# Performance work log

Measured on AMD Instinct MI355X. Metric: run time of the kernel, lower is better.

The kernel has to match this reference:

```python
import jax, jax.numpy as jnp
import numpy as np
from jax.scipy.special import digamma

K_NEIGHBOURS = 5  # matches init_kwargs nNeighbours


def setup_inputs() -> dict:
    key = jax.random.key(0)
    k1, k2 = jax.random.split(key)
    x = jax.random.normal(k1, (2, 2, 64, 64), dtype=jnp.float32)
    y = jax.random.normal(k2, (2, 2, 64, 64), dtype=jnp.float32)
    return {"x": x, "y": y}


def _knn_mi(x, y, k):
    # KSG k-NN mutual information estimator, channel-wise.
    B, C, H, W = x.shape
    BC, HW = B * C, H * W
    xv = x.reshape(BC, HW)
    yv = y.reshape(BC, HW)
    # Pairwise L1 (scalar -> abs diff) distance matrices: (BC, HW, HW)
    dx = jnp.abs(xv[:, :, None] - xv[:, None, :])
    dy = jnp.abs(yv[:, :, None] - yv[:, None, :])
    # Joint-space Chebyshev distance (max over the two marginals)
    z = jnp.maximum(dx, dy)
    # eps = (k+1)-th smallest joint distance per point (includes self-distance 0),
    # matching torch .topk(k+1, largest=False).values[..., -1:]
    neg_smallest = jax.lax.top_k(-z, k + 1)[0]       # (BC, HW, k+1), descending in -z
    eps = -neg_smallest[:, :, -1:]                    # (BC, HW, 1)
    # Marginal neighbor counts with strict < eps (self included, as in torch code)
    nx = jnp.sum(dx < eps, axis=-1).astype(jnp.float32)  # (BC, HW)
    ny = jnp.sum(dy < eps, axis=-1).astype(jnp.float32)
    const = digamma(jnp.float32(k)) + digamma(jnp.float32(HW))
    mi = const - jnp.mean(digamma(nx) + digamma(ny), axis=-1)  # (BC,)
    return jnp.maximum(mi.reshape(B, C), 0.0)


def reference(x, y):
    return _knn_mi(x, y, K_NEIGHBOURS)
```

## Files before the change

### kernel.cpp

```cpp
#include <hip/hip_runtime.h>
#include <math.h>

#define HW 4096
#define NCH 4
#define TPB 256
#define ROWS_PER_BLOCK 16
#define BLOCKS_PER_CH 256
#define NBLOCKS (NCH * BLOCKS_PER_CH)
#define KNN 5
#define WIN 512

#define NBINS 512
#define BLO   (-6.0f)
#define BDELTA 0.0234375f
#define BINV  (512.0f / 12.0f)
#define SLOP  1e-5f
#define INFT  3.4e38f

#define WS_BXY   16384
#define WS_BY    32768
#define WS_PREF  49152
#define WS_PART  57344

__device__ __forceinline__ int binOf(float v) {
    int b = (int)floorf((v - BLO) * BINV);
    return min(max(b, 0), NBINS - 1);
}

__device__ __forceinline__ float digammaf_dev(float x) {
    float r = 0.f;
    while (x < 6.f) { r -= 1.f / x; x += 1.f; }
    float f = 1.f / x, f2 = f * f;
    return logf(x) - 0.5f * f
         - f2 * (1.f / 12.f - f2 * (1.f / 120.f - f2 * (1.f / 252.f))) + r;
}

__device__ __forceinline__ void insert6(float (&s)[6], float d) {
    float n0 = fminf(s[0], d);
    float n1 = __builtin_amdgcn_fmed3f(s[0], s[1], d);
    float n2 = __builtin_amdgcn_fmed3f(s[1], s[2], d);
    float n3 = __builtin_amdgcn_fmed3f(s[2], s[3], d);
    float n4 = __builtin_amdgcn_fmed3f(s[3], s[4], d);
    float n5 = __builtin_amdgcn_fmed3f(s[4], s[5], d);
    s[0] = n0; s[1] = n1; s[2] = n2; s[3] = n3; s[4] = n4; s[5] = n5;
}

__global__ __launch_bounds__(256) void knnmi_bucketize(const float* __restrict__ x,
                                                       const float* __restrict__ y,
                                                       float* __restrict__ ws) {
    __shared__ int h[NBINS];
    const int c    = blockIdx.x >> 1;
    const int side = blockIdx.x & 1;
    const int t    = threadIdx.x;
    const float* src  = (side == 0 ? x : y) + c * HW;
    const float* ysrc = y + c * HW;
    int* pref = (int*)ws + WS_PREF + (side ? NCH * (NBINS + 1) : 0) + c * (NBINS + 1);

    for (int i = t; i < NBINS; i += 256) h[i] = 0;
    __syncthreads();

    float vx[16], vy[16];
    int bn[16];
#pragma unroll
    for (int k = 0; k < 16; ++k) {
        int i = t + k * 256;
        float v = src[i];
        vx[k] = v;
        vy[k] = (side == 0) ? ysrc[i] : 0.f;
        bn[k] = binOf(v);
        atomicAdd(&h[bn[k]], 1);
    }
    __syncthreads();

    if (t < 64) {
        int sinc[8];
        {
            int c0 = h[t * 8 + 0];
            sinc[0] = c0;
#pragma unroll
            for (int j = 1; j < 8; ++j) sinc[j] = sinc[j - 1] + h[t * 8 + j];
        }
        int tot = sinc[7], inc = tot;
#pragma unroll
        for (int off = 1; off < 64; off <<= 1) {
            int u = __shfl_up(inc, off);
            if (t >= off) inc += u;
        }
        int ex = inc - tot;
#pragma unroll
        for (int j = 0; j < 8; ++j) {
            int st = ex + (j ? sinc[j - 1] : 0);
            h[t * 8 + j]    = st;
            pref[t * 8 + j] = st;
        }
        if (t == 63) pref[NBINS] = HW;
    }
    __syncthreads();

    if (side == 0) {
        float* bxx = ws + c * HW;
        float* bxy = ws + WS_BXY + c * HW;
#pragma unroll
        for (int k = 0; k < 16; ++k) {
            int pos = atomicAdd(&h[bn[k]], 1);
            bxx[pos] = vx[k];
            bxy[pos] = vy[k];
        }
    } else {
        float* by = ws + WS_BY + c * HW;
#pragma unroll
        for (int k = 0; k < 16; ++k) {
            int pos = atomicAdd(&h[bn[k]], 1);
            by[pos] = vx[k];
        }
    }
}

__global__ __launch_bounds__(TPB) void knnmi_rows(float* __restrict__ ws) {
    __shared__ float2 sxy[HW];
    __shared__ float  ys[HW];
    __shared__ int pfx[NBINS + 1], pfy[NBINS + 1];
    __shared__ float red[ROWS_PER_BLOCK];

    const int c  = blockIdx.x >> 8;
    const int rb = blockIdx.x & 255;
    const float* bxx = ws + c * HW;
    const float* bxy = ws + WS_BXY + c * HW;
    const float* by  = ws + WS_BY  + c * HW;
    const int* prefx = (const int*)ws + WS_PREF + c * (NBINS + 1);
    const int* prefy = (const int*)ws + WS_PREF + NCH * (NBINS + 1) + c * (NBINS + 1);

    for (int i = threadIdx.x; i < HW / 4; i += TPB) {
        float4 xv = ((const float4*)bxx)[i];
        float4 yv = ((const float4*)bxy)[i];
        ((float4*)sxy)[2 * i]     = make_float4(xv.x, yv.x, xv.y, yv.y);
        ((float4*)sxy)[2 * i + 1] = make_float4(xv.z, yv.z, xv.w, yv.w);
        ((float4*)ys)[i] = ((const float4*)by)[i];
    }
    for (int i = threadIdx.x; i <= NBINS; i += TPB) {
        pfx[i] = prefx[i];
        pfy[i] = prefy[i];
    }
    __syncthreads();

    const int wv   = threadIdx.x >> 6;
    const int lane = threadIdx.x & 63;
    const int l    = lane & 15;
    const int g    = lane >> 4;
    const int q    = wv * 4 + g;
    const int p    = rb + 256 * q;

    const float xi = sxy[p].x;
    const float yi = sxy[p].y;

    int lo = p - WIN / 2;
    lo = max(lo, 0); lo = min(lo, HW - WIN); lo &= ~1;
    const int hi = lo + WIN;
    const float4* f4 = (const float4*)sxy;
    const int fbase = lo >> 1;

    float s[6];
#pragma unroll
    for (int k = 0; k < 6; ++k) s[k] = INFT;

#pragma unroll 8
    for (int it = 0; it < WIN / 32; ++it) {
        float4 pp = f4[fbase + it * 16 + l];
        insert6(s, fmaxf(fabsf(xi - pp.x), fabsf(yi - pp.y)));
        insert6(s, fmaxf(fabsf(xi - pp.z), fabsf(yi - pp.w)));
    }

#pragma unroll
    for (int m = 1; m < 16; m <<= 1) {
        float o[6];
#pragma unroll
        for (int k = 0; k < 6; ++k) o[k] = __shfl_xor(s[k], m);
#pragma unroll
        for (int k = 0; k < 6; ++k) insert6(s, o[k]);
    }
    float eps = s[5];

    float eL = INFT, eR = INFT;
    if (lo > 0) {
        int b = binOf(sxy[lo - 1].x);
        eL = xi - (BLO + (float)(b + 1) * BDELTA + SLOP);
    }
    if (hi < HW) {
        int b = binOf(sxy[hi].x);
        eR = (BLO + (float)b * BDELTA - SLOP) - xi;
    }
    const bool ok = (eps <= eL) && (eps <= eR);

    unsigned long long bad = __ballot((l == 0) && !ok);
    while (bad) {
        int bit = (int)__ffsll((unsigned long long)bad) - 1;
        bad &= bad - 1;
        const int tg = bit >> 4;
        const int pt = rb + 256 * (wv * 4 + tg);
        const float xt = sxy[pt].x, yt = sxy[pt].y;
        float s3[6];
#pragma unroll
        for (int k = 0; k < 6; ++k) s3[k] = INFT;
#pragma unroll 8
        for (int it = 0; it < HW / 128; ++it) {
            float4 pp = f4[it * 64 + lane];
            insert6(s3, fmaxf(fabsf(xt - pp.x), fabsf(yt - pp.y)));
            insert6(s3, fmaxf(fabsf(xt - pp.z), fabsf(yt - pp.w)));
        }
#pragma unroll
        for (int m = 1; m < 64; m <<= 1) {
            float o[6];
#pragma unroll
            for (int k = 0; k < 6; ++k) o[k] = __shfl_xor(s3[k], m);
#pragma unroll
            for (int k = 0; k < 6; ++k) insert6(s3, o[k]);
        }
        if (g == tg) eps = s3[5];
    }

    int nx = 0;
    {
        int loB = binOf(xi - eps), hiB = binOf(xi + eps);
        int fLo = loB + 2, fHi = hiB - 2;
        if (fLo <= fHi) {
            if (l == 0) nx += pfx[fHi + 1] - pfx[fLo];
            int a0 = pfx[max(loB - 1, 0)], a1 = pfx[min(loB + 1, NBINS - 1) + 1];
            int b0 = pfx[max(hiB - 1, 0)], b1 = pfx[min(hiB + 1, NBINS - 1) + 1];
            for (int tt = a0 + l; tt < a1; tt += 16) nx += (fabsf(sxy[tt].x - xi) < eps);
            for (int tt = b0 + l; tt < b1; tt += 16) nx += (fabsf(sxy[tt].x - xi) < eps);
        } else {
            int a0 = pfx[max(loB - 1, 0)], a1 = pfx[min(hiB + 1, NBINS - 1) + 1];
            for (int tt = a0 + l; tt < a1; tt += 16) nx += (fabsf(sxy[tt].x - xi) < eps);
        }
    }
    int ny = 0;
    {
        int loB = binOf(yi - eps), hiB = binOf(yi + eps);
        int fLo = loB + 2, fHi = hiB - 2;
        if (fLo <= fHi) {
            if (l == 0) ny += pfy[fHi + 1] - pfy[fLo];
            int a0 = pfy[max(loB - 1, 0)], a1 = pfy[min(loB + 1, NBINS - 1) + 1];
            int b0 = pfy[max(hiB - 1, 0)], b1 = pfy[min(hiB + 1, NBINS - 1) + 1];
            for (int tt = a0 + l; tt < a1; tt += 16) ny += (fabsf(ys[tt] - yi) < eps);
            for (int tt = b0 + l; tt < b1; tt += 16) ny += (fabsf(ys[tt] - yi) < eps);
        } else {
            int a0 = pfy[max(loB - 1, 0)], a1 = pfy[min(hiB + 1, NBINS - 1) + 1];
            for (int tt = a0 + l; tt < a1; tt += 16) ny += (fabsf(ys[tt] - yi) < eps);
        }
    }

    int pk = (nx << 16) | ny;
#pragma unroll
    for (int m = 1; m < 16; m <<= 1) pk += __shfl_xor(pk, m);

    if (l == 0)
        red[q] = digammaf_dev((float)(pk >> 16)) + digammaf_dev((float)(pk & 0xffff));
    __syncthreads();

    if (threadIdx.x == 0) {
        float v = 0.f;
#pragma unroll
        for (int k = 0; k < ROWS_PER_BLOCK; ++k) v += red[k];
        (ws + WS_PART)[blockIdx.x] = v;
    }
}

__global__ void knnmi_final(const float* __restrict__ ws, float* __restrict__ out) {
    const float* partials = ws + WS_PART;
    const int w    = threadIdx.x >> 6;
    const int lane = threadIdx.x & 63;
    float sum = 0.f;
#pragma unroll
    for (int i = lane; i < BLOCKS_PER_CH; i += 64)
        sum += partials[w * BLOCKS_PER_CH + i];
#pragma unroll
    for (int m = 32; m; m >>= 1) sum += __shfl_xor(sum, m);
    if (lane == 0) {
        float mi = digammaf_dev((float)KNN) + digammaf_dev((float)HW)
                 - sum / (float)HW;
        out[w] = fmaxf(mi, 0.f);
    }
}

extern "C" void kernel_launch(void* const* d_in, const int* in_sizes, int n_in,
                              void* d_out, int out_size, void* d_ws, size_t ws_size,
                              hipStream_t stream) {
    const float* x = (const float*)d_in[0];
    const float* y = (const float*)d_in[1];
    float* out = (float*)d_out;
    float* ws  = (float*)d_ws;

    knnmi_bucketize<<<2 * NCH, 256, 0, stream>>>(x, y, ws);
    knnmi_rows<<<NBLOCKS, TPB, 0, stream>>>(ws);
    knnmi_final<<<1, NCH * 64, 0, stream>>>(ws, out);
}
```

Baseline: 32.84 us.

## Assign contiguous row blocks and stage only a shared local window in LDS

Each block now handles 16 consecutive sorted rows instead of strided rows. It therefore loads only a 544-element shared window into LDS, rather than the full 4096-point channel plus the y array and prefix tables. The marginal counting and the full-scan fallback now read global memory (L2-cached) directly. This removes the large per-block LDS fill and raises occupancy (launch bounds 6), at the cost of uncached global reads in the counting loops.

```diff
diff --git a/kernel.cpp b/kernel.cpp
--- a/kernel.cpp
+++ b/kernel.cpp
@@ -8,7 +8,7 @@
 #define BLOCKS_PER_CH 256
 #define NBLOCKS (NCH * BLOCKS_PER_CH)
 #define KNN 5
-#define WIN 512
+#define WINB 544
 
 #define NBINS 512
 #define BLO   (-6.0f)
@@ -75,8 +75,7 @@
     if (t < 64) {
         int sinc[8];
         {
-            int c0 = h[t * 8 + 0];
-            sinc[0] = c0;
+            sinc[0] = h[t * 8 + 0];
 #pragma unroll
             for (int j = 1; j < 8; ++j) sinc[j] = sinc[j - 1] + h[t * 8 + j];
         }
@@ -116,30 +115,28 @@
     }
 }
 
-__global__ __launch_bounds__(TPB) void knnmi_rows(float* __restrict__ ws) {
-    __shared__ float2 sxy[HW];
-    __shared__ float  ys[HW];
-    __shared__ int pfx[NBINS + 1], pfy[NBINS + 1];
+__global__ __launch_bounds__(TPB, 6) void knnmi_rows(float* __restrict__ ws) {
+    __shared__ float2 swin[WINB];
     __shared__ float red[ROWS_PER_BLOCK];
 
     const int c  = blockIdx.x >> 8;
     const int rb = blockIdx.x & 255;
+    const int R0 = rb * ROWS_PER_BLOCK;
     const float* bxx = ws + c * HW;
     const float* bxy = ws + WS_BXY + c * HW;
     const float* by  = ws + WS_BY  + c * HW;
-    const int* prefx = (const int*)ws + WS_PREF + c * (NBINS + 1);
-    const int* prefy = (const int*)ws + WS_PREF + NCH * (NBINS + 1) + c * (NBINS + 1);
-
-    for (int i = threadIdx.x; i < HW / 4; i += TPB) {
-        float4 xv = ((const float4*)bxx)[i];
-        float4 yv = ((const float4*)bxy)[i];
-        ((float4*)sxy)[2 * i]     = make_float4(xv.x, yv.x, xv.y, yv.y);
-        ((float4*)sxy)[2 * i + 1] = make_float4(xv.z, yv.z, xv.w, yv.w);
-        ((float4*)ys)[i] = ((const float4*)by)[i];
-    }
-    for (int i = threadIdx.x; i <= NBINS; i += TPB) {
-        pfx[i] = prefx[i];
-        pfy[i] = prefy[i];
+    const int* pfx = (const int*)ws + WS_PREF + c * (NBINS + 1);
+    const int* pfy = (const int*)ws + WS_PREF + NCH * (NBINS + 1) + c * (NBINS + 1);
+
+    int LO = R0 - 256;
+    LO = max(LO, 0); LO = min(LO, HW - WINB); LO &= ~3;
+    const int HI = LO + WINB;
+
+    if (threadIdx.x < WINB / 4) {
+        float4 xv = ((const float4*)(bxx + LO))[threadIdx.x];
+        float4 yv = ((const float4*)(bxy + LO))[threadIdx.x];
+        ((float4*)swin)[2 * threadIdx.x]     = make_float4(xv.x, yv.x, xv.y, yv.y);
+        ((float4*)swin)[2 * threadIdx.x + 1] = make_float4(xv.z, yv.z, xv.w, yv.w);
     }
     __syncthreads();
 
@@ -148,24 +145,19 @@
     const int l    = lane & 15;
     const int g    = lane >> 4;
     const int q    = wv * 4 + g;
-    const int p    = rb + 256 * q;
-
-    const float xi = sxy[p].x;
-    const float yi = sxy[p].y;
-
-    int lo = p - WIN / 2;
-    lo = max(lo, 0); lo = min(lo, HW - WIN); lo &= ~1;
-    const int hi = lo + WIN;
-    const float4* f4 = (const float4*)sxy;
-    const int fbase = lo >> 1;
+    const int p    = R0 + q;
+
+    const float xi = swin[p - LO].x;
+    const float yi = swin[p - LO].y;
 
     float s[6];
 #pragma unroll
     for (int k = 0; k < 6; ++k) s[k] = INFT;
 
-#pragma unroll 8
-    for (int it = 0; it < WIN / 32; ++it) {
-        float4 pp = f4[fbase + it * 16 + l];
+    const float4* f4 = (const float4*)swin;
+#pragma unroll 4
+    for (int it = 0; it < WINB / 32; ++it) {
+        float4 pp = f4[it * 16 + l];
         insert6(s, fmaxf(fabsf(xi - pp.x), fabsf(yi - pp.y)));
         insert6(s, fmaxf(fabsf(xi - pp.z), fabsf(yi - pp.w)));
     }
@@ -181,12 +173,12 @@
     float eps = s[5];
 
     float eL = INFT, eR = INFT;
-    if (lo > 0) {
-        int b = binOf(sxy[lo - 1].x);
+    if (LO > 0) {
+        int b = binOf(bxx[LO - 1]);
         eL = xi - (BLO + (float)(b + 1) * BDELTA + SLOP);
     }
-    if (hi < HW) {
-        int b = binOf(sxy[hi].x);
+    if (HI < HW) {
+        int b = binOf(bxx[HI]);
         eR = (BLO + (float)b * BDELTA - SLOP) - xi;
     }
     const bool ok = (eps <= eL) && (eps <= eR);
@@ -196,16 +188,18 @@
         int bit = (int)__ffsll((unsigned long long)bad) - 1;
         bad &= bad - 1;
         const int tg = bit >> 4;
-        const int pt = rb + 256 * (wv * 4 + tg);
-        const float xt = sxy[pt].x, yt = sxy[pt].y;
+        const int pt = R0 + wv * 4 + tg;
+        const float xt = swin[pt - LO].x, yt = swin[pt - LO].y;
         float s3[6];
 #pragma unroll
         for (int k = 0; k < 6; ++k) s3[k] = INFT;
-#pragma unroll 8
-        for (int it = 0; it < HW / 128; ++it) {
-            float4 pp = f4[it * 64 + lane];
-            insert6(s3, fmaxf(fabsf(xt - pp.x), fabsf(yt - pp.y)));
-            insert6(s3, fmaxf(fabsf(xt - pp.z), fabsf(yt - pp.w)));
+        for (int it = 0; it < HW / 256; ++it) {
+            float4 xv = ((const float4*)bxx)[it * 64 + lane];
+            float4 yv = ((const float4*)bxy)[it * 64 + lane];
+            insert6(s3, fmaxf(fabsf(xt - xv.x), fabsf(yt - yv.x)));
+            insert6(s3, fmaxf(fabsf(xt - xv.y), fabsf(yt - yv.y)));
+            insert6(s3, fmaxf(fabsf(xt - xv.z), fabsf(yt - yv.z)));
+            insert6(s3, fmaxf(fabsf(xt - xv.w), fabsf(yt - yv.w)));
         }
 #pragma unroll
         for (int m = 1; m < 64; m <<= 1) {
@@ -226,11 +220,11 @@
             if (l == 0) nx += pfx[fHi + 1] - pfx[fLo];
             int a0 = pfx[max(loB - 1, 0)], a1 = pfx[min(loB + 1, NBINS - 1) + 1];
             int b0 = pfx[max(hiB - 1, 0)], b1 = pfx[min(hiB + 1, NBINS - 1) + 1];
-            for (int tt = a0 + l; tt < a1; tt += 16) nx += (fabsf(sxy[tt].x - xi) < eps);
-            for (int tt = b0 + l; tt < b1; tt += 16) nx += (fabsf(sxy[tt].x - xi) < eps);
+            for (int tt = a0 + l; tt < a1; tt += 16) nx += (fabsf(bxx[tt] - xi) < eps);
+            for (int tt = b0 + l; tt < b1; tt += 16) nx += (fabsf(bxx[tt] - xi) < eps);
         } else {
             int a0 = pfx[max(loB - 1, 0)], a1 = pfx[min(hiB + 1, NBINS - 1) + 1];
-            for (int tt = a0 + l; tt < a1; tt += 16) nx += (fabsf(sxy[tt].x - xi) < eps);
+            for (int tt = a0 + l; tt < a1; tt += 16) nx += (fabsf(bxx[tt] - xi) < eps);
         }
     }
     int ny = 0;
@@ -241,11 +235,11 @@
             if (l == 0) ny += pfy[fHi + 1] - pfy[fLo];
             int a0 = pfy[max(loB - 1, 0)], a1 = pfy[min(loB + 1, NBINS - 1) + 1];
             int b0 = pfy[max(hiB - 1, 0)], b1 = pfy[min(hiB + 1, NBINS - 1) + 1];
-            for (int tt = a0 + l; tt < a1; tt += 16) ny += (fabsf(ys[tt] - yi) < eps);
-            for (int tt = b0 + l; tt < b1; tt += 16) ny += (fabsf(ys[tt] - yi) < eps);
+            for (int tt = a0 + l; tt < a1; tt += 16) ny += (fabsf(by[tt] - yi) < eps);
+            for (int tt = b0 + l; tt < b1; tt += 16) ny += (fabsf(by[tt] - yi) < eps);
         } else {
             int a0 = pfy[max(loB - 1, 0)], a1 = pfy[min(hiB + 1, NBINS - 1) + 1];
-            for (int tt = a0 + l; tt < a1; tt += 16) ny += (fabsf(ys[tt] - yi) < eps);
+            for (int tt = a0 + l; tt < a1; tt += 16) ny += (fabsf(by[tt] - yi) < eps);
         }
     }
 
```

New measurement: 31.01 us. -5.6%, faster.
